# Kernel optimization log

Hardware: AMD Instinct MI355X
Metric: run time of the kernel (lower is better)

## Reference

```python
import jax, jax.numpy as jnp
import numpy as np

N = 80000       # nodes
E = 1280000     # edges (avg degree 16)
G = 2000        # graphs
NSHAPE, NCOLOR, POSMAX = 16, 16, 1024
HID, OUT, IN_DIM = 64, 2, 40
EPS = 1e-5


def setup_inputs() -> dict:
    key = jax.random.key(0)
    ks = jax.random.split(key, 20)
    f32 = jnp.float32
    return {
        "shape_id": jax.random.randint(ks[0], (N,), 0, NSHAPE),
        "color_id": jax.random.randint(ks[1], (N,), 0, NCOLOR),
        "pos_id": jax.random.randint(ks[2], (N,), 0, POSMAX),
        "edge_index": jax.random.randint(ks[3], (2, E), 0, N),
        "batch": jnp.sort(jax.random.randint(ks[4], (N,), 0, G)),
        "num_graphs": G,
        "shape_tab": jax.random.normal(ks[5], (NSHAPE, 16), f32),
        "color_tab": jax.random.normal(ks[6], (NCOLOR, 16), f32),
        "pos_tab": jax.random.normal(ks[7], (POSMAX, 8), f32),
        "W1l": jax.random.normal(ks[8], (IN_DIM, HID), f32) / np.sqrt(IN_DIM),
        "b1": jnp.zeros((HID,), f32),
        "W1r": jax.random.normal(ks[9], (IN_DIM, HID), f32) / np.sqrt(IN_DIM),
        "g1": jnp.ones((HID,), f32),
        "be1": jnp.zeros((HID,), f32),
        "W2l": jax.random.normal(ks[10], (HID, HID), f32) / np.sqrt(HID),
        "b2": jnp.zeros((HID,), f32),
        "W2r": jax.random.normal(ks[11], (HID, HID), f32) / np.sqrt(HID),
        "g2": jnp.ones((HID,), f32),
        "be2": jnp.zeros((HID,), f32),
        "Wout": jax.random.normal(ks[12], (HID, OUT), f32) / np.sqrt(HID),
        "bout": jnp.zeros((OUT,), f32),
    }


def sage_conv(x, src, dst, Wl, b, Wr, n_nodes):
    # PyG SAGEConv (mean aggr): out = lin_l(mean_{j in N(i)} x_j) + lin_r(x_i)
    agg = jax.ops.segment_sum(x[src], dst, num_segments=n_nodes)     # [N, F]
    deg = jax.ops.segment_sum(jnp.ones((src.shape[0], 1), x.dtype), dst,
                              num_segments=n_nodes)                  # [N, 1]
    agg = agg / jnp.maximum(deg, 1.0)
    return agg @ Wl + b + x @ Wr


def batch_norm(x, gamma, beta):
    # training-mode BatchNorm1d over nodes
    m = x.mean(axis=0)
    v = x.var(axis=0)
    return (x - m) * (gamma / jnp.sqrt(v + EPS)) + beta


def reference(shape_id, color_id, pos_id, edge_index, batch, num_graphs,
              shape_tab, color_tab, pos_tab,
              W1l, b1, W1r, g1, be1,
              W2l, b2, W2r, g2, be2,
              Wout, bout):
    n_nodes = shape_id.shape[0]
    src, dst = edge_index[0], edge_index[1]
    x = jnp.concatenate([shape_tab[shape_id], color_tab[color_id],
                         pos_tab[pos_id]], axis=-1)                  # [N, 40]
    x = jax.nn.relu(batch_norm(sage_conv(x, src, dst, W1l, b1, W1r, n_nodes), g1, be1))
    # dropout: eval mode -> identity
    x = jax.nn.relu(batch_norm(sage_conv(x, src, dst, W2l, b2, W2r, n_nodes), g2, be2))
    # global mean pool over batch segments
    summed = jax.ops.segment_sum(x, batch, num_segments=num_graphs)   # [G, H]
    counts = jax.ops.segment_sum(jnp.ones((n_nodes, 1), x.dtype), batch,
                                 num_segments=num_graphs)
    pooled = summed / jnp.maximum(counts, 1.0)
    return pooled @ Wout + bout                                       # [G, 2]
```

## Files before the change

### kernel.cpp

```cpp
#include <hip/hip_runtime.h>

#define NN 80000
#define NE 1280000
#define NG 2000
#define HID 64
#define FIN1 40
#define BSZ 128
#define NBUK (NN / BSZ)
#define EB 8192
#define NBB ((NE + EB - 1) / EB)
#define NBBP 160
constexpr float EPS = 1e-5f;

typedef _Float16 f16;
typedef f16 f16x8 __attribute__((ext_vector_type(8)));
typedef float f32x4 __attribute__((ext_vector_type(4)));

__global__ void setup2(const int* __restrict__ sid, const int* __restrict__ cid,
                       const int* __restrict__ pid, const int* __restrict__ batch,
                       const float* __restrict__ stab, const float* __restrict__ ctab,
                       const float* __restrict__ ptab,
                       const float* __restrict__ W1l, const float* __restrict__ W1r,
                       const float* __restrict__ W2l, const float* __restrict__ W2r,
                       const int* __restrict__ dst,
                       int* __restrict__ ids, f16* __restrict__ Bt1, f16* __restrict__ Bt2,
                       int* __restrict__ gstart,
                       f16* __restrict__ stab16, f16* __restrict__ ctab16,
                       f16* __restrict__ ptab16,
                       float* __restrict__ stats,
                       int* __restrict__ bhistT) {
    __shared__ int lh[NBUK];
    int bid = blockIdx.x;
    int tid = threadIdx.x;
    if (bid < 313) {
        int n = bid * 256 + tid;
        if (n < NN) ids[n] = sid[n] | (cid[n] << 4) | (pid[n] << 8);
    } else if (bid < 373) {
        int i = (bid - 313) * 256 + tid;
        if (i < 64 * 104) {
            int j = i / 104, k = i - j * 104;
            float v = 0.f;
            if (k < 40) v = W1l[k * 64 + j];
            else if (k < 80) v = W1r[(k - 40) * 64 + j];
            Bt1[i] = (f16)v;
        }
        int i2 = i - 64 * 104;
        if (i2 >= 0 && i2 < 64 * 136) {
            int j = i2 / 136, k = i2 - j * 136;
            float v = 0.f;
            if (k < 64) v = W2l[k * 64 + j];
            else if (k < 128) v = W2r[(k - 64) * 64 + j];
            Bt2[i2] = (f16)v;
        }
    } else if (bid < 686) {
        int n = (bid - 373) * 256 + tid;
        if (n >= NN) return;
        int cur = batch[n];
        int prev = (n == 0) ? -1 : batch[n - 1];
        for (int g = prev + 1; g <= cur; g++) gstart[g] = n;
        if (n == NN - 1)
            for (int g = cur + 1; g <= NG; g++) gstart[g] = NN;
    } else if (bid < 720) {
        int i = (bid - 686) * 256 + tid;
        if (i < 256) stab16[i] = (f16)stab[i];
        else if (i < 512) ctab16[i - 256] = (f16)ctab[i - 256];
        else if (i < 512 + 8192) ptab16[i - 512] = (f16)ptab[i - 512];
    } else if (bid == 720) {
        if (tid < 256) stats[tid] = 0.f;
    } else {
        int kb = bid - 721;
        for (int i = tid; i < NBUK; i += 256) lh[i] = 0;
        __syncthreads();
        int e0 = kb * EB, e1 = min(e0 + EB, NE);
        for (int e = e0 + tid; e < e1; e += 256) atomicAdd(&lh[dst[e] >> 7], 1);
        __syncthreads();
        for (int i = tid; i < NBUK; i += 256) bhistT[i * NBBP + kb] = lh[i];
    }
}

__global__ void kscan(const int* __restrict__ bhistT, int* __restrict__ bstart,
                      int* __restrict__ lbaseT) {
    __shared__ int redA[256];
    __shared__ int s0s;
    int b = blockIdx.x, t = threadIdx.x;
    int s = 0;
    for (int i = t; i < b; i += 256) {
        const int* rowp = &bhistT[i * NBBP];
        int cs = 0;
        for (int blk = 0; blk < NBB; blk++) cs += rowp[blk];
        s += cs;
    }
    redA[t] = s;
    __syncthreads();
    for (int off = 128; off >= 1; off >>= 1) {
        if (t < off) redA[t] += redA[t + off];
        __syncthreads();
    }
    if (t == 0) {
        bstart[b] = redA[0];
        if (b == 0) bstart[NBUK] = NE;
        s0s = redA[0];
    }
    __syncthreads();
    if (t < 64) {
        int run = s0s;
        for (int i0 = 0; i0 < NBB; i0 += 64) {
            int idx = i0 + t;
            int v = (idx < NBB) ? bhistT[b * NBBP + idx] : 0;
            int inc = v;
#pragma unroll
            for (int off = 1; off < 64; off <<= 1) {
                int tt2 = __shfl_up(inc, off);
                if (t >= off) inc += tt2;
            }
            if (idx < NBB) lbaseT[b * NBBP + idx] = run + inc - v;
            run += __shfl(inc, 63);
        }
    }
}

__global__ void kbin(const int* __restrict__ src, const int* __restrict__ dst,
                     const int* __restrict__ lbaseT, int* __restrict__ ebuf) {
    __shared__ int lcur[NBUK];
    for (int i = threadIdx.x; i < NBUK; i += 256) lcur[i] = lbaseT[i * NBBP + blockIdx.x];
    __syncthreads();
    int e0 = blockIdx.x * EB, e1 = min(e0 + EB, NE);
    for (int e = e0 + threadIdx.x; e < e1; e += 256) {
        int d = dst[e];
        int off = atomicAdd(&lcur[d >> 7], 1);
        ebuf[off] = (src[e] << 7) | (d & 127);
    }
}

__global__ void kfill(const int* __restrict__ ebuf, const int* __restrict__ bstart,
                      int* __restrict__ row_ptr, int* __restrict__ eidx) {
    __shared__ int cnt[BSZ];
    __shared__ int sb[BSZ];
    __shared__ int lcur[BSZ];
    int b = blockIdx.x, t = threadIdx.x;
    int nbase = b << 7;
    if (t < BSZ) cnt[t] = 0;
    __syncthreads();
    int s0 = bstart[b], s1 = bstart[b + 1];
    for (int i = s0 + t; i < s1; i += 256) atomicAdd(&cnt[ebuf[i] & 127], 1);
    __syncthreads();
    if (t < BSZ) sb[t] = cnt[t];
    __syncthreads();
    for (int off = 1; off < BSZ; off <<= 1) {
        int v = (t >= off && t < BSZ) ? sb[t - off] : 0;
        __syncthreads();
        if (t < BSZ) sb[t] += v;
        __syncthreads();
    }
    if (t < BSZ) {
        int excl = ((t == 0) ? 0 : sb[t - 1]) + s0;
        row_ptr[nbase + t] = excl;
        lcur[t] = excl;
    }
    if (b == 0 && t == 0) row_ptr[NN] = NE;
    __syncthreads();
    for (int i = s0 + t; i < s1; i += 256) {
        int v = ebuf[i];
        int pos = atomicAdd(&lcur[v & 127], 1);
        eidx[pos] = v >> 7;
    }
}

__global__ void gather1(const int* __restrict__ row_ptr, const int* __restrict__ eidx,
                        const int* __restrict__ ids,
                        const f16* __restrict__ stab16, const f16* __restrict__ ctab16,
                        const f16* __restrict__ ptab16, f16* __restrict__ agg) {
    int tt = blockIdx.x * 256 + threadIdx.x;
    int n = tt >> 6;
    int lane = threadIdx.x & 63;
    if (n >= NN) return;
    int grp = lane >> 3, li = lane & 7;
    bool act = li < 5;
    int beg = row_ptr[n], end = row_ptr[n + 1];
    f16x8 ach;
#pragma unroll
    for (int i = 0; i < 8; i++) ach[i] = (f16)0.f;
    for (int j0 = beg; j0 < end; j0 += 64) {
        int cnt = min(64, end - j0);
        int myid = (j0 + lane < end) ? eidx[j0 + lane] : 0;
        int steps = (cnt + 7) >> 3;
        for (int u = 0; u < steps; u++) {
            int e = u * 8 + grp;
            int s = __shfl(myid, e);
            if (e < cnt && act) {
                int id = ids[s];
                const f16* rowp;
                if (li < 2)      rowp = &stab16[(id & 15) * 16 + li * 8];
                else if (li < 4) rowp = &ctab16[((id >> 4) & 15) * 16 + (li - 2) * 8];
                else             rowp = &ptab16[(id >> 8) * 8];
                ach += *(const f16x8*)rowp;
            }
        }
    }
    float ac[8];
#pragma unroll
    for (int i = 0; i < 8; i++) ac[i] = (float)ach[i];
#pragma unroll
    for (int m = 8; m <= 32; m <<= 1) {
#pragma unroll
        for (int i = 0; i < 8; i++) ac[i] += __shfl_xor(ac[i], m);
    }
    if (lane < 5) {
        float inv = 1.0f / (float)max(end - beg, 1);
        f16x8 o;
#pragma unroll
        for (int i = 0; i < 8; i++) o[i] = (f16)(ac[i] * inv);
        *(f16x8*)&agg[(size_t)n * FIN1 + lane * 8] = o;
    }
}

__global__ void bn_apply16(f16* __restrict__ h, const float* __restrict__ stats,
                           const float* __restrict__ g, const float* __restrict__ be) {
    __shared__ float ssc[64], ssh[64];
    int tid = threadIdx.x;
    if (tid < 64) {
        const float invn = 1.0f / (float)NN;
        float m = stats[tid] * invn;
        float var = stats[64 + tid] * invn - m * m;
        float sc = g[tid] * __frsqrt_rn(var + EPS);
        ssc[tid] = sc;
        ssh[tid] = be[tid] - m * sc;
    }
    __syncthreads();
    int idx = blockIdx.x * 256 + tid;
    if (idx >= NN * 8) return;
    int f = (idx & 7) * 8;
    f16x8 v = *(f16x8*)&h[(size_t)idx * 8];
    f16x8 o;
#pragma unroll
    for (int i = 0; i < 8; i++) {
        float xv = (float)v[i];
        o[i] = (f16)fmaxf(fmaf(xv, ssc[f + i], ssh[f + i]), 0.f);
    }
    *(f16x8*)&h[(size_t)idx * 8] = o;
}

__global__ void gather2(const int* __restrict__ row_ptr, const int* __restrict__ eidx,
                        const f16* __restrict__ x, f16* __restrict__ agg) {
    int tt = blockIdx.x * 256 + threadIdx.x;
    int n = tt >> 6;
    int lane = threadIdx.x & 63;
    if (n >= NN) return;
    int grp = lane >> 3;
    int fl = (lane & 7) * 8;
    int beg = row_ptr[n], end = row_ptr[n + 1];
    f16x8 ach;
#pragma unroll
    for (int i = 0; i < 8; i++) ach[i] = (f16)0.f;
    for (int j0 = beg; j0 < end; j0 += 64) {
        int cnt = min(64, end - j0);
        int myid = (j0 + lane < end) ? eidx[j0 + lane] : 0;
        int steps = (cnt + 7) >> 3;
        for (int u = 0; u < steps; u++) {
            int e = u * 8 + grp;
            int s = __shfl(myid, e);
            if (e < cnt) {
                ach += *(const f16x8*)&x[(size_t)s * HID + fl];
            }
        }
    }
    float ac[8];
#pragma unroll
    for (int i = 0; i < 8; i++) ac[i] = (float)ach[i];
#pragma unroll
    for (int m = 8; m <= 32; m <<= 1) {
#pragma unroll
        for (int i = 0; i < 8; i++) ac[i] += __shfl_xor(ac[i], m);
    }
    if (lane < 8) {
        float inv = 1.0f / (float)max(end - beg, 1);
        f16x8 o;
#pragma unroll
        for (int i = 0; i < 8; i++) o[i] = (f16)(ac[i] * inv);
        *(f16x8*)&agg[(size_t)n * HID + fl] = o;
    }
}

__launch_bounds__(256)
__global__ void sage_mfma1(const int* __restrict__ ids, const f16* __restrict__ aggv,
                           const f16* __restrict__ stab16, const f16* __restrict__ ctab16,
                           const f16* __restrict__ ptab16,
                           const f16* __restrict__ Btg, const float* __restrict__ bias,
                           f16* __restrict__ h, float* __restrict__ stats) {
    __shared__ float sred[4][64];
    __shared__ float qred[4][64];
    const int KP = 104;

    int tid = threadIdx.x;
    int n0 = blockIdx.x * 64;
    int w = tid >> 6, l = tid & 63;
    int jloc = l & 15, kg = l >> 4;
    int n = n0 + w * 16 + jloc;

    f16x8 af[3];
#pragma unroll
    for (int kk = 0; kk < 3; kk++) {
        int c = kk * 4 + kg;
        if (c < 5) {
            af[kk] = *(const f16x8*)&aggv[(size_t)n * FIN1 + c * 8];
        } else if (c < 10) {
            int id = ids[n];
            int cc = c - 5;
            const f16* rowp;
            if (cc < 2)      rowp = &stab16[(id & 15) * 16 + cc * 8];
            else if (cc < 4) rowp = &ctab16[((id >> 4) & 15) * 16 + (cc - 2) * 8];
            else             rowp = &ptab16[(id >> 8) * 8];
            af[kk] = *(const f16x8*)rowp;
        } else {
#pragma unroll
            for (int i = 0; i < 8; i++) af[kk][i] = (f16)0.f;
        }
    }

    f32x4 acc[4];
#pragma unroll
    for (int jt = 0; jt < 4; jt++) {
        float bj = bias[jt * 16 + jloc];
        acc[jt] = (f32x4){bj, bj, bj, bj};
    }
#pragma unroll
    for (int kk = 0; kk < 3; kk++) {
#pragma unroll
        for (int jt = 0; jt < 4; jt++) {
            f16x8 bf = *(const f16x8*)&Btg[(jt * 16 + jloc) * KP + kk * 32 + kg * 8];
            acc[jt] = __builtin_amdgcn_mfma_f32_16x16x32_f16(af[kk], bf, acc[jt], 0, 0, 0);
        }
    }
#pragma unroll
    for (int jt = 0; jt < 4; jt++) {
        float sv = 0.f, qv = 0.f;
#pragma unroll
        for (int reg = 0; reg < 4; reg++) {
            f16 hv = (f16)acc[jt][reg];
            int nn2 = n0 + w * 16 + kg * 4 + reg;
            h[(size_t)nn2 * HID + jt * 16 + jloc] = hv;
            float v = (float)hv;
            sv += v; qv += v * v;
        }
        sv += __shfl_xor(sv, 16); sv += __shfl_xor(sv, 32);
        qv += __shfl_xor(qv, 16); qv += __shfl_xor(qv, 32);
        if (kg == 0) { sred[w][jt * 16 + jloc] = sv; qred[w][jt * 16 + jloc] = qv; }
    }
    __syncthreads();
    if (tid < 128) {
        int f2 = tid & 63, which = tid >> 6;
        float r = which ? (qred[0][f2] + qred[1][f2] + qred[2][f2] + qred[3][f2])
                        : (sred[0][f2] + sred[1][f2] + sred[2][f2] + sred[3][f2]);
        atomicAdd(&stats[which * 64 + f2], r);
    }
}

__launch_bounds__(256)
__global__ void sage_mfma2(const f16* __restrict__ x, const f16* __restrict__ aggv,
                           const f16* __restrict__ Btg, const float* __restrict__ bias,
                           f16* __restrict__ h, float* __restrict__ stats) {
    __shared__ float sred[4][64];
    __shared__ float qred[4][64];
    const int KP = 136;

    int tid = threadIdx.x;
    int n0 = blockIdx.x * 64;
    int w = tid >> 6, l = tid & 63;
    int jloc = l & 15, kg = l >> 4;
    int n = n0 + w * 16 + jloc;

    f16x8 af[4];
#pragma unroll
    for (int kk = 0; kk < 4; kk++) {
        int c = kk * 4 + kg;
        if (c < 8) af[kk] = *(const f16x8*)&aggv[(size_t)n * HID + c * 8];
        else       af[kk] = *(const f16x8*)&x[(size_t)n * HID + (c - 8) * 8];
    }

    f32x4 acc[4];
#pragma unroll
    for (int jt = 0; jt < 4; jt++) {
        float bj = bias[jt * 16 + jloc];
        acc[jt] = (f32x4){bj, bj, bj, bj};
    }
#pragma unroll
    for (int kk = 0; kk < 4; kk++) {
#pragma unroll
        for (int jt = 0; jt < 4; jt++) {
            f16x8 bf = *(const f16x8*)&Btg[(jt * 16 + jloc) * KP + kk * 32 + kg * 8];
            acc[jt] = __builtin_amdgcn_mfma_f32_16x16x32_f16(af[kk], bf, acc[jt], 0, 0, 0);
        }
    }
#pragma unroll
    for (int jt = 0; jt < 4; jt++) {
        float sv = 0.f, qv = 0.f;
#pragma unroll
        for (int reg = 0; reg < 4; reg++) {
            f16 hv = (f16)acc[jt][reg];
            int nn2 = n0 + w * 16 + kg * 4 + reg;
            h[(size_t)nn2 * HID + jt * 16 + jloc] = hv;
            float v = (float)hv;
            sv += v; qv += v * v;
        }
        sv += __shfl_xor(sv, 16); sv += __shfl_xor(sv, 32);
        qv += __shfl_xor(qv, 16); qv += __shfl_xor(qv, 32);
        if (kg == 0) { sred[w][jt * 16 + jloc] = sv; qred[w][jt * 16 + jloc] = qv; }
    }
    __syncthreads();
    if (tid < 128) {
        int f2 = tid & 63, which = tid >> 6;
        float r = which ? (qred[0][f2] + qred[1][f2] + qred[2][f2] + qred[3][f2])
                        : (sred[0][f2] + sred[1][f2] + sred[2][f2] + sred[3][f2]);
        atomicAdd(&stats[which * 64 + f2], r);
    }
}

__global__ void pool_out(const f16* __restrict__ h, const float* __restrict__ stats2,
                         const float* __restrict__ g2, const float* __restrict__ be2,
                         const int* __restrict__ gstart,
                         const float* __restrict__ Wout, const float* __restrict__ bout,
                         float* __restrict__ out) {
    __shared__ float red[4][64];
    int w = blockIdx.x;
    int tid = threadIdx.x;
    int f = tid & 63, seg = tid >> 6;
    const float invn = 1.0f / (float)NN;
    float m = stats2[f] * invn;
    float var = stats2[64 + f] * invn - m * m;
    float sc = g2[f] / sqrtf(var + EPS);
    float sh = be2[f] - m * sc;
    int n0 = gstart[w], n1 = gstart[w + 1];
    float acc = 0.f;
    for (int n = n0 + seg; n < n1; n += 4) {
        float v = fmaf((float)h[(size_t)n * HID + f], sc, sh);
        acc += fmaxf(v, 0.0f);
    }
    red[seg][f] = acc;
    __syncthreads();
    if (seg == 0) {
        acc = red[0][f] + red[1][f] + red[2][f] + red[3][f];
        float inv = 1.0f / (float)max(n1 - n0, 1);
        float p = acc * inv;
        float a0 = p * Wout[f * 2 + 0];
        float a1 = p * Wout[f * 2 + 1];
#pragma unroll
        for (int mm = 1; mm < 64; mm <<= 1) {
            a0 += __shfl_xor(a0, mm);
            a1 += __shfl_xor(a1, mm);
        }
        if (f == 0) {
            out[w * 2 + 0] = a0 + bout[0];
            out[w * 2 + 1] = a1 + bout[1];
        }
    }
}

extern "C" void kernel_launch(void* const* d_in, const int* in_sizes, int n_in,
                              void* d_out, int out_size, void* d_ws, size_t ws_size,
                              hipStream_t stream) {
    const int* sid = (const int*)d_in[0];
    const int* cid = (const int*)d_in[1];
    const int* pid = (const int*)d_in[2];
    const int* ei = (const int*)d_in[3];
    const int* batch = (const int*)d_in[4];
    const float* stab = (const float*)d_in[6];
    const float* ctab = (const float*)d_in[7];
    const float* ptab = (const float*)d_in[8];
    const float* W1l = (const float*)d_in[9];
    const float* b1 = (const float*)d_in[10];
    const float* W1r = (const float*)d_in[11];
    const float* g1 = (const float*)d_in[12];
    const float* be1 = (const float*)d_in[13];
    const float* W2l = (const float*)d_in[14];
    const float* b2 = (const float*)d_in[15];
    const float* W2r = (const float*)d_in[16];
    const float* g2 = (const float*)d_in[17];
    const float* be2 = (const float*)d_in[18];
    const float* Wout = (const float*)d_in[19];
    const float* bout = (const float*)d_in[20];

    const int* src = ei;
    const int* dst = ei + NE;

    char* p = (char*)d_ws;
    f16* agg = (f16*)p;        p += (size_t)NN * HID * 2;
    f16* h1 = (f16*)p;         p += (size_t)NN * HID * 2;
    f16* h2 = (f16*)p;         p += (size_t)NN * HID * 2;
    f16* bt1 = (f16*)p;        p += 64 * 104 * 2;
    f16* bt2 = (f16*)p;        p += 64 * 136 * 2;
    f16* stab16 = (f16*)p;     p += 256 * 2;
    f16* ctab16 = (f16*)p;     p += 256 * 2;
    f16* ptab16 = (f16*)p;     p += 8192 * 2;
    float* stats = (float*)p;  p += 256 * 4;
    int* ids = (int*)p;        p += (size_t)NN * 4;
    int* row_ptr = (int*)p;    p += (NN + 1) * 4;
    int* gstart = (int*)p;     p += (NG + 1) * 4;
    int* bstart = (int*)p;     p += (NBUK + 1) * 4;
    int* bhistT = (int*)p;     p += (size_t)NBUK * NBBP * 4;
    int* lbaseT = (int*)p;     p += (size_t)NBUK * NBBP * 4;
    int* ebuf = (int*)p;       p += (size_t)NE * 4;
    int* eidx = (int*)p;       p += (size_t)NE * 4;

    const int B = 256;

    setup2<<<721 + NBB, B, 0, stream>>>(sid, cid, pid, batch, stab, ctab, ptab,
                                        W1l, W1r, W2l, W2r, dst,
                                        ids, bt1, bt2, gstart, stab16, ctab16, ptab16,
                                        stats, bhistT);

    kscan<<<NBUK, B, 0, stream>>>(bhistT, bstart, lbaseT);
    kbin<<<NBB, B, 0, stream>>>(src, dst, lbaseT, ebuf);
    kfill<<<NBUK, B, 0, stream>>>(ebuf, bstart, row_ptr, eidx);

    gather1<<<(NN * 64 + B - 1) / B, B, 0, stream>>>(row_ptr, eidx, ids,
                                                     stab16, ctab16, ptab16, agg);
    sage_mfma1<<<NN / 64, B, 0, stream>>>(ids, agg, stab16, ctab16, ptab16,
                                          bt1, b1, h1, stats);
    bn_apply16<<<(NN * 8 + B - 1) / B, B, 0, stream>>>(h1, stats, g1, be1);

    gather2<<<(NN * 64 + B - 1) / B, B, 0, stream>>>(row_ptr, eidx, h1, agg);
    sage_mfma2<<<NN / 64, B, 0, stream>>>(h1, agg, bt2, b2, h2, stats + 128);

    pool_out<<<NG, B, 0, stream>>>(h2, stats + 128, g2, be2, gstart,
                                   Wout, bout, (float*)d_out);
}
```

Measured before the change: 226.1 us.

## Split bucket scan into single-block prefix scan plus per-bucket local scan

```diff
diff --git a/kernel.cpp b/kernel.cpp
--- a/kernel.cpp
+++ b/kernel.cpp
@@ -78,44 +78,42 @@
     }
 }
 
-__global__ void kscan(const int* __restrict__ bhistT, int* __restrict__ bstart,
-                      int* __restrict__ lbaseT) {
-    __shared__ int redA[256];
-    __shared__ int s0s;
-    int b = blockIdx.x, t = threadIdx.x;
-    int s = 0;
-    for (int i = t; i < b; i += 256) {
-        const int* rowp = &bhistT[i * NBBP];
-        int cs = 0;
+__global__ void kscanA(const int* __restrict__ bhistT, int* __restrict__ bstart) {
+    __shared__ int l[1024];
+    int t = threadIdx.x;
+    int cs = 0;
+    if (t < NBUK) {
+        const int* rowp = &bhistT[t * NBBP];
         for (int blk = 0; blk < NBB; blk++) cs += rowp[blk];
-        s += cs;
-    }
-    redA[t] = s;
-    __syncthreads();
-    for (int off = 128; off >= 1; off >>= 1) {
-        if (t < off) redA[t] += redA[t + off];
+    }
+    l[t] = cs;
+    __syncthreads();
+    for (int off = 1; off < 1024; off <<= 1) {
+        int v = (t >= off) ? l[t - off] : 0;
         __syncthreads();
-    }
-    if (t == 0) {
-        bstart[b] = redA[0];
-        if (b == 0) bstart[NBUK] = NE;
-        s0s = redA[0];
-    }
-    __syncthreads();
-    if (t < 64) {
-        int run = s0s;
-        for (int i0 = 0; i0 < NBB; i0 += 64) {
-            int idx = i0 + t;
-            int v = (idx < NBB) ? bhistT[b * NBBP + idx] : 0;
-            int inc = v;
-#pragma unroll
-            for (int off = 1; off < 64; off <<= 1) {
-                int tt2 = __shfl_up(inc, off);
-                if (t >= off) inc += tt2;
-            }
-            if (idx < NBB) lbaseT[b * NBBP + idx] = run + inc - v;
-            run += __shfl(inc, 63);
-        }
+        l[t] += v;
+        __syncthreads();
+    }
+    if (t < NBUK) bstart[t] = (t == 0) ? 0 : l[t - 1];
+    if (t == NBUK) bstart[NBUK] = NE;
+}
+
+__global__ void kscanB(const int* __restrict__ bhistT, const int* __restrict__ bstart,
+                       int* __restrict__ lbaseT) {
+    int b = blockIdx.x;
+    int l = threadIdx.x;
+    int run = bstart[b];
+    for (int i0 = 0; i0 < NBB; i0 += 64) {
+        int idx = i0 + l;
+        int v = (idx < NBB) ? bhistT[b * NBBP + idx] : 0;
+        int inc = v;
+#pragma unroll
+        for (int off = 1; off < 64; off <<= 1) {
+            int tt = __shfl_up(inc, off);
+            if (l >= off) inc += tt;
+        }
+        if (idx < NBB) lbaseT[b * NBBP + idx] = run + inc - v;
+        run += __shfl(inc, 63);
     }
 }
 
@@ -508,7 +506,8 @@
                                         ids, bt1, bt2, gstart, stab16, ctab16, ptab16,
                                         stats, bhistT);
 
-    kscan<<<NBUK, B, 0, stream>>>(bhistT, bstart, lbaseT);
+    kscanA<<<1, 1024, 0, stream>>>(bhistT, bstart);
+    kscanB<<<NBUK, 64, 0, stream>>>(bhistT, bstart, lbaseT);
     kbin<<<NBB, B, 0, stream>>>(src, dst, lbaseT, ebuf);
     kfill<<<NBUK, B, 0, stream>>>(ebuf, bstart, row_ptr, eidx);
 
```

Measured after the change: 223.3 us. Within noise of the previous version (-1.3%).
